# Kernel optimization log

Measured on AMD Instinct MI355X. Metric: run time of the kernel, lower is better.

The kernel has to match this reference:

```python
import jax, jax.numpy as jnp
import numpy as np
from jax import lax

B, T, U, V = 4, 200, 100, 1024
D_ENC, D_DEC, J = 144, 320, 320


def setup_inputs() -> dict:
    key = jax.random.key(0)
    ks = jax.random.split(key, 8)
    s = lambda d: 1.0 / np.sqrt(d).astype(np.float32)
    return {
        "enc_out": jax.random.normal(ks[0], (B, T, D_ENC), jnp.float32),
        "dec_out": jax.random.normal(ks[1], (B, U + 1, D_DEC), jnp.float32),
        "W_enc": jax.random.normal(ks[2], (D_ENC, J), jnp.float32) * s(D_ENC),
        "b_enc": jnp.zeros((J,), jnp.float32),
        "W_dec": jax.random.normal(ks[3], (D_DEC, J), jnp.float32) * s(D_DEC),
        "b_dec": jnp.zeros((J,), jnp.float32),
        "W_out": jax.random.normal(ks[4], (J, V), jnp.float32) * s(J),
        "b_out": jnp.zeros((V,), jnp.float32),
        "targets": jax.random.randint(ks[5], (B, U), 1, V, jnp.int32),
        "enc_lengths": jax.random.randint(ks[6], (B,), T // 2, T + 1, jnp.int32),
        "target_lengths": jax.random.randint(ks[7], (B,), U // 2, U + 1, jnp.int32),
    }


def _rnnt_loss(log_probs, targets, enc_lengths, target_lengths):
    # log_probs: [B, T, U+1, V]; blank index = 0 (matches RNNTLoss(blank=0))
    blank_lp = log_probs[..., 0]  # [B, T, U+1]
    idx = jnp.broadcast_to(targets[:, None, :, None].astype(jnp.int32), (B, T, U, 1))
    emit_lp = jnp.take_along_axis(log_probs[:, :, :U, :], idx, axis=-1)[..., 0]  # [B, T, U]

    # alpha[0, u] = sum of emit log-probs along u at t=0
    alpha0 = jnp.concatenate(
        [jnp.zeros((B, 1), log_probs.dtype), jnp.cumsum(emit_lp[:, 0, :], axis=1)], axis=1
    )  # [B, U+1]

    def row(a, emit_t):
        # a: alpha_prev + blank (vertical transitions), [B, U+1]; emit_t: [B, U]
        def step(prev, xs):
            a_u, e_prev = xs
            cur = jnp.logaddexp(a_u, prev + e_prev)
            return cur, cur
        _, rest = lax.scan(step, a[:, 0], (a[:, 1:].T, emit_t.T))  # rest: [U, B]
        return jnp.concatenate([a[:, :1], rest.T], axis=1)

    def t_step(alpha_prev, xs):
        blank_prev, emit_t = xs
        alpha_t = row(alpha_prev + blank_prev, emit_t)
        return alpha_t, alpha_t

    xs = (jnp.swapaxes(blank_lp[:, :-1, :], 0, 1), jnp.swapaxes(emit_lp[:, 1:, :], 0, 1))
    _, alphas_rest = lax.scan(t_step, alpha0, xs)  # [T-1, B, U+1]
    alphas = jnp.concatenate([alpha0[None], alphas_rest], axis=0)  # [T, B, U+1]

    b_idx = jnp.arange(B)
    t_idx = enc_lengths - 1
    ll = alphas[t_idx, b_idx, target_lengths] + blank_lp[b_idx, t_idx, target_lengths]
    return jnp.mean(-ll)  # reduction='mean' over batch


def reference(enc_out, dec_out, W_enc, b_enc, W_dec, b_dec, W_out, b_out, targets, enc_lengths, target_lengths):
    enc_p = enc_out @ W_enc + b_enc  # [B, T, J]
    dec_p = dec_out @ W_dec + b_dec  # [B, U+1, J]
    joint = jnp.tanh(enc_p[:, :, None, :] + dec_p[:, None, :, :])  # [B, T, U+1, J]
    logits = joint @ W_out + b_out  # [B, T, U+1, V]
    log_probs = jax.nn.log_softmax(logits, axis=-1)
    return _rnnt_loss(log_probs, targets, enc_lengths, target_lengths)
```

## Files before the change

kernel.cpp:

```cpp
#include <hip/hip_runtime.h>
#include <hip/hip_bf16.h>
#include <math.h>

#define B_ 4
#define T_ 200
#define U_ 100
#define V_ 1024
#define DE 144
#define DD 320
#define J_ 320
#define M_TOT (B_ * T_ * (U_ + 1))
#define SSTR 328
#define DSTR 104
#define NDIAG 300
#define LOG2E 1.4426950408889634f
#define LN2 0.6931471805599453f

typedef __attribute__((ext_vector_type(8))) short bf16x8_t;
typedef __attribute__((ext_vector_type(4))) float f32x4_t;

__device__ __forceinline__ float fast_tanh(float x) {
    float e = exp2f(x * (2.0f * LOG2E));
    float r = __frcp_rn(e + 1.0f);
    return fmaf(-2.0f, r, 1.0f);
}

__device__ __forceinline__ ushort f2bf(float x) {
    uint u = __float_as_uint(x);
    uint r = (u + 0x7FFFu + ((u >> 16) & 1u)) >> 16;
    return (ushort)r;
}

template <int K>
__device__ __forceinline__ void proj_body(const float* __restrict__ X,
                                          const float* __restrict__ W,
                                          const float* __restrict__ bias,
                                          float* __restrict__ Y,
                                          int r0, int R, float* sx, int tid) {
    constexpr int QK = K / 4;
    for (int q = tid; q < 16 * QK; q += 640) {
        int row = q / QK;
        int kq = q - row * QK;
        int r = r0 + row;
        if (r >= R) r = R - 1;
        *(float4*)&sx[row * K + kq * 4] = *(const float4*)&X[r * K + kq * 4];
    }
    __syncthreads();
    const int half = (tid >= 320) ? 1 : 0;
    const int c = tid - half * 320;
    float acc[8];
#pragma unroll
    for (int i = 0; i < 8; i++) acc[i] = 0.0f;
    for (int k = 0; k < K; k += 4) {
        float w0 = W[(k + 0) * 320 + c];
        float w1 = W[(k + 1) * 320 + c];
        float w2 = W[(k + 2) * 320 + c];
        float w3 = W[(k + 3) * 320 + c];
#pragma unroll
        for (int i = 0; i < 8; i++) {
            const float4 x4 = *(const float4*)&sx[(half * 8 + i) * K + k];
            acc[i] = fmaf(x4.x, w0, acc[i]);
            acc[i] = fmaf(x4.y, w1, acc[i]);
            acc[i] = fmaf(x4.z, w2, acc[i]);
            acc[i] = fmaf(x4.w, w3, acc[i]);
        }
    }
    const float bb = bias[c];
#pragma unroll
    for (int i = 0; i < 8; i++) {
        int r = r0 + half * 8 + i;
        if (r < R) Y[r * 320 + c] = acc[i] + bb;
    }
}

__global__ __launch_bounds__(640) void prep_kernel(
    const float* __restrict__ enc_out, const float* __restrict__ dec_out,
    const float* __restrict__ W_enc, const float* __restrict__ b_enc,
    const float* __restrict__ W_dec, const float* __restrict__ b_dec,
    const float* __restrict__ W_out,
    float* __restrict__ enc_p, float* __restrict__ dec_p,
    ushort* __restrict__ Wt) {
    __shared__ float sx[16 * 320];
    const int bid = blockIdx.x;
    const int tid = threadIdx.x;
    if (bid < 50) {
        proj_body<DE>(enc_out, W_enc, b_enc, enc_p, bid * 16, B_ * T_, sx, tid);
    } else if (bid < 76) {
        proj_body<DD>(dec_out, W_dec, b_dec, dec_p, (bid - 50) * 16,
                      B_ * (U_ + 1), sx, tid);
    } else {
        int idx = (bid - 76) * 640 + tid;
        int k = idx >> 10;
        int v = idx & 1023;
        ushort b = f2bf(W_out[idx]);
        int frag = (v >> 4) * 10 + (k >> 5);
        int lane = (v & 15) | (((k >> 3) & 3) << 4);
        int elem = k & 7;
        Wt[frag * 512 + lane * 8 + elem] = b;
    }
}

__global__ __launch_bounds__(1024, 4) void joint_mfma(
    const float* __restrict__ enc_p, const float* __restrict__ dec_p,
    const ushort* __restrict__ Wt, const float* __restrict__ b_out,
    const int* __restrict__ targets,
    float* __restrict__ bsk, float* __restrict__ esk) {
    __shared__ ushort sh[64 * SSTR];
    __shared__ float parts[16][64];
    __shared__ float lse_sh[64];
    __shared__ int tgt_sh[64];
    __shared__ int skb_sh[64];

    const int tid = threadIdx.x;
    const int r0 = blockIdx.x * 64;

    if (tid < 64) {
        int rc = r0 + tid;
        int tg = -1, skb = -1;
        if (rc < M_TOT) {
            int b = rc / 20200;
            int rem = rc - b * 20200;
            int t = rem / 101;
            int u = rem - t * 101;
            skb = (b * NDIAG + t + u) * DSTR + u;
            if (u < U_) tg = targets[b * U_ + u];
        }
        tgt_sh[tid] = tg;
        skb_sh[tid] = skb;
    }

    {
        const int si = tid >> 4;
        const int sq = tid & 15;
        int rc = r0 + si;
        if (rc > M_TOT - 1) rc = M_TOT - 1;
        int b = rc / 20200;
        int rem = rc - b * 20200;
        int t = rem / 101;
        int u = rem - t * 101;
        const float4* ep = (const float4*)&enc_p[(b * 200 + t) * 320];
        const float4* dp = (const float4*)&dec_p[(b * 101 + u) * 320];
        ushort* shp = &sh[si * SSTR];
#pragma unroll
        for (int it = 0; it < 5; it++) {
            int kq = sq + it * 16;
            float4 e = ep[kq];
            float4 dd = dp[kq];
            float t0 = fast_tanh(e.x + dd.x);
            float t1 = fast_tanh(e.y + dd.y);
            float t2 = fast_tanh(e.z + dd.z);
            float t3 = fast_tanh(e.w + dd.w);
            __hip_bfloat162 p0 = __float22bfloat162_rn(make_float2(t0, t1));
            __hip_bfloat162 p1 = __float22bfloat162_rn(make_float2(t2, t3));
            uint2 pk;
            pk.x = *(uint*)&p0;
            pk.y = *(uint*)&p1;
            *(uint2*)&shp[kq * 4] = pk;
        }
    }
    __syncthreads();

    const int wave = tid >> 6;
    const int lane = tid & 63;
    const int lrow = lane & 15;
    const int lk = (lane >> 4) * 8;
    const int cb16 = wave * 4;

    f32x4_t acc[4][4];
#pragma unroll
    for (int mt = 0; mt < 4; mt++)
#pragma unroll
        for (int nt = 0; nt < 4; nt++) acc[mt][nt] = (f32x4_t)(0.0f);

    for (int ks = 0; ks < 10; ks++) {
        bf16x8_t a[4];
#pragma unroll
        for (int mt = 0; mt < 4; mt++)
            a[mt] = *(const bf16x8_t*)&sh[(mt * 16 + lrow) * SSTR + ks * 32 + lk];
#pragma unroll
        for (int nt = 0; nt < 4; nt++) {
            bf16x8_t bfr = *(const bf16x8_t*)&Wt[(((cb16 + nt) * 10 + ks) << 9) + lane * 8];
            __builtin_amdgcn_s_setprio(1);
#pragma unroll
            for (int mt = 0; mt < 4; mt++)
                acc[mt][nt] = __builtin_amdgcn_mfma_f32_16x16x32_bf16(a[mt], bfr, acc[mt][nt], 0, 0, 0);
            __builtin_amdgcn_s_setprio(0);
        }
    }

    float bo[4];
#pragma unroll
    for (int nt = 0; nt < 4; nt++) bo[nt] = b_out[wave * 64 + nt * 16 + lrow];
#pragma unroll
    for (int mt = 0; mt < 4; mt++)
#pragma unroll
        for (int nt = 0; nt < 4; nt++) acc[mt][nt] += bo[nt];

#pragma unroll
    for (int mt = 0; mt < 4; mt++) {
#pragma unroll
        for (int j = 0; j < 4; j++) {
            float s = exp2f(acc[mt][0][j] * LOG2E);
            s += exp2f(acc[mt][1][j] * LOG2E);
            s += exp2f(acc[mt][2][j] * LOG2E);
            s += exp2f(acc[mt][3][j] * LOG2E);
#pragma unroll
            for (int off = 1; off < 16; off <<= 1)
                s += __shfl_xor(s, off, 16);
            if (lrow == 0) {
                int row = mt * 16 + (lane >> 4) * 4 + j;
                parts[wave][row] = s;
            }
        }
    }
    __syncthreads();
    if (tid < 64) {
        float s = parts[0][tid];
#pragma unroll
        for (int w = 1; w < 16; w++) s += parts[w][tid];
        lse_sh[tid] = __log2f(s) * LN2;
    }
    __syncthreads();

#pragma unroll
    for (int mt = 0; mt < 4; mt++) {
#pragma unroll
        for (int j = 0; j < 4; j++) {
            int lr = mt * 16 + (lane >> 4) * 4 + j;
            int skb = skb_sh[lr];
            if (skb < 0) continue;
            int tc = tgt_sh[lr];
            bool isblank = (wave == 0) && (lrow == 0);
            bool isemit = (tc >= 0) && ((tc >> 6) == wave) && ((tc & 15) == lrow);
            if (isblank || isemit) {
                float lse = lse_sh[lr];
                if (isblank) bsk[skb] = acc[mt][0][j] - lse;
                if (isemit) {
                    int ntl = (tc >> 4) & 3;
                    float v = acc[mt][0][j];
#pragma unroll
                    for (int nt = 1; nt < 4; nt++)
                        if (nt == ntl) v = acc[mt][nt][j];
                    esk[skb] = v - lse;
                }
            }
        }
    }
}

__global__ __launch_bounds__(256, 1) void alpha_c2_kernel(
    const float* __restrict__ bsk, const float* __restrict__ esk,
    const int* __restrict__ enc_len, const int* __restrict__ tgt_len,
    float* __restrict__ out) {
    __shared__ float ll_sh[B_];
    const int tid = threadIdx.x;
    const int b = tid >> 6;
    const int l = tid & 63;
    const float* Bp = bsk + b * (NDIAG * DSTR);
    const float* Ep = esk + b * (NDIAG * DSTR);
    const int el = enc_len[b];
    const int tl = tgt_len[b];
    const int dfin = el - 1 + tl;

    const int u0 = 2 * l;
    const bool ok0 = (u0 <= U_);
    const bool ok1 = (u0 + 1 <= U_);
    const int uc = ok0 ? u0 : 0;

    float A0 = (l == 0) ? 0.0f : -INFINITY;
    float A1 = -INFINITY;

    float2 rb[16], re[16];
#pragma unroll
    for (int k = 0; k < 16; k++) {
        rb[k] = *(const float2*)&Bp[k * DSTR + uc];
        re[k] = *(const float2*)&Ep[k * DSTR + uc];
    }

    for (int dc = 1; dc <= 289; dc += 16) {
#pragma unroll
        for (int q = 0; q < 16; q++) {
            const int d = dc + q;
            if (d > NDIAG - 1) continue;
            const int sc = q;
            const int sm = (q + 1) & 15;
            float2 cb = rb[sc], ce = re[sc];
            float2 mb = rb[sm];
            int dn = d + 15;
            if (dn > NDIAG - 1) dn = NDIAG - 1;
            rb[sc] = *(const float2*)&Bp[dn * DSTR + uc];
            re[sc] = *(const float2*)&Ep[dn * DSTR + uc];

            float s = A1 + ce.y;
            float sn = __shfl_up(s, 1, 64);

            float va0 = A0 + cb.x;
            float vb0 = (l >= 1) ? sn : -INFINITY;
            float va1 = A1 + cb.y;
            float vb1 = A0 + ce.x;

            float M0 = fmaxf(va0, vb0);
            float n0 = (M0 == -INFINITY)
                           ? -INFINITY
                           : M0 + __logf(1.0f + __expf(fminf(va0, vb0) - M0));
            float M1 = fmaxf(va1, vb1);
            float n1 = (M1 == -INFINITY)
                           ? -INFINITY
                           : M1 + __logf(1.0f + __expf(fminf(va1, vb1) - M1));

            const int t0 = d - u0;
            if (!ok0 || t0 < 0 || t0 >= T_) n0 = -INFINITY;
            if (!ok1 || (t0 - 1) < 0 || (t0 - 1) >= T_) n1 = -INFINITY;

            if (d == dfin) {
                if (tl == u0) ll_sh[b] = n0 + mb.x;
                if (tl == u0 + 1) ll_sh[b] = n1 + mb.y;
            }
            A0 = n0;
            A1 = n1;
        }
    }
    __syncthreads();
    if (tid == 0)
        out[0] = -0.25f * (ll_sh[0] + ll_sh[1] + ll_sh[2] + ll_sh[3]);
}

extern "C" void kernel_launch(void* const* d_in, const int* in_sizes, int n_in,
                              void* d_out, int out_size, void* d_ws, size_t ws_size,
                              hipStream_t stream) {
    const float* enc_out = (const float*)d_in[0];
    const float* dec_out = (const float*)d_in[1];
    const float* W_enc = (const float*)d_in[2];
    const float* b_enc = (const float*)d_in[3];
    const float* W_dec = (const float*)d_in[4];
    const float* b_dec = (const float*)d_in[5];
    const float* W_out = (const float*)d_in[6];
    const float* b_out = (const float*)d_in[7];
    const int* targets = (const int*)d_in[8];
    const int* enc_len = (const int*)d_in[9];
    const int* tgt_len = (const int*)d_in[10];

    float* ws = (float*)d_ws;
    float* enc_p = ws;
    float* dec_p = enc_p + B_ * T_ * J_;
    float* bsk = dec_p + B_ * (U_ + 1) * J_;
    float* esk = bsk + B_ * NDIAG * DSTR;
    ushort* Wt = (ushort*)(esk + B_ * NDIAG * DSTR);

    prep_kernel<<<588, 640, 0, stream>>>(enc_out, dec_out, W_enc, b_enc,
                                         W_dec, b_dec, W_out, enc_p, dec_p, Wt);

    joint_mfma<<<(M_TOT + 63) / 64, 1024, 0, stream>>>(
        enc_p, dec_p, Wt, b_out, targets, bsk, esk);

    alpha_c2_kernel<<<1, 256, 0, stream>>>(bsk, esk, enc_len, tgt_len,
                                           (float*)d_out);
}
```

Measured before the change: 204.4 us.

## Fuse prep, joint GEMM and alpha recursion into one cooperative persistent kernel

Replaces three kernel launches with a single cooperative kernel of 256 persistent blocks. Grid syncs separate the projection/weight-conversion phase, a grid-stride loop over joint GEMM tiles, and the alpha recursion run by one block. It also folds the output bias into the exp2 FMA argument. The aim is to remove launch overhead and inter-kernel gaps. In exchange, the GEMM phase runs at only 256 blocks, which may lower occupancy, and the grid-wide barriers add their own cost.

```diff
diff --git a/kernel.cpp b/kernel.cpp
--- a/kernel.cpp
+++ b/kernel.cpp
@@ -1,6 +1,9 @@
 #include <hip/hip_runtime.h>
 #include <hip/hip_bf16.h>
+#include <hip/hip_cooperative_groups.h>
 #include <math.h>
+
+namespace cg = cooperative_groups;
 
 #define B_ 4
 #define T_ 200
@@ -10,6 +13,7 @@
 #define DD 320
 #define J_ 320
 #define M_TOT (B_ * T_ * (U_ + 1))
+#define NTILES 1263
 #define SSTR 328
 #define DSTR 104
 #define NDIAG 300
@@ -31,298 +35,293 @@
     return (ushort)r;
 }
 
-template <int K>
-__device__ __forceinline__ void proj_body(const float* __restrict__ X,
-                                          const float* __restrict__ W,
-                                          const float* __restrict__ bias,
-                                          float* __restrict__ Y,
-                                          int r0, int R, float* sx, int tid) {
-    constexpr int QK = K / 4;
-    for (int q = tid; q < 16 * QK; q += 640) {
-        int row = q / QK;
-        int kq = q - row * QK;
-        int r = r0 + row;
-        if (r >= R) r = R - 1;
-        *(float4*)&sx[row * K + kq * 4] = *(const float4*)&X[r * K + kq * 4];
-    }
-    __syncthreads();
-    const int half = (tid >= 320) ? 1 : 0;
-    const int c = tid - half * 320;
-    float acc[8];
-#pragma unroll
-    for (int i = 0; i < 8; i++) acc[i] = 0.0f;
-    for (int k = 0; k < K; k += 4) {
-        float w0 = W[(k + 0) * 320 + c];
-        float w1 = W[(k + 1) * 320 + c];
-        float w2 = W[(k + 2) * 320 + c];
-        float w3 = W[(k + 3) * 320 + c];
-#pragma unroll
-        for (int i = 0; i < 8; i++) {
-            const float4 x4 = *(const float4*)&sx[(half * 8 + i) * K + k];
-            acc[i] = fmaf(x4.x, w0, acc[i]);
-            acc[i] = fmaf(x4.y, w1, acc[i]);
-            acc[i] = fmaf(x4.z, w2, acc[i]);
-            acc[i] = fmaf(x4.w, w3, acc[i]);
-        }
-    }
-    const float bb = bias[c];
-#pragma unroll
-    for (int i = 0; i < 8; i++) {
-        int r = r0 + half * 8 + i;
-        if (r < R) Y[r * 320 + c] = acc[i] + bb;
-    }
-}
-
-__global__ __launch_bounds__(640) void prep_kernel(
+__global__ __launch_bounds__(1024, 4) void fused_kernel(
     const float* __restrict__ enc_out, const float* __restrict__ dec_out,
     const float* __restrict__ W_enc, const float* __restrict__ b_enc,
     const float* __restrict__ W_dec, const float* __restrict__ b_dec,
-    const float* __restrict__ W_out,
+    const float* __restrict__ W_out, const float* __restrict__ b_out,
+    const int* __restrict__ targets, const int* __restrict__ enc_len,
+    const int* __restrict__ tgt_len,
     float* __restrict__ enc_p, float* __restrict__ dec_p,
-    ushort* __restrict__ Wt) {
-    __shared__ float sx[16 * 320];
-    const int bid = blockIdx.x;
-    const int tid = threadIdx.x;
-    if (bid < 50) {
-        proj_body<DE>(enc_out, W_enc, b_enc, enc_p, bid * 16, B_ * T_, sx, tid);
-    } else if (bid < 76) {
-        proj_body<DD>(dec_out, W_dec, b_dec, dec_p, (bid - 50) * 16,
-                      B_ * (U_ + 1), sx, tid);
-    } else {
-        int idx = (bid - 76) * 640 + tid;
-        int k = idx >> 10;
-        int v = idx & 1023;
-        ushort b = f2bf(W_out[idx]);
-        int frag = (v >> 4) * 10 + (k >> 5);
-        int lane = (v & 15) | (((k >> 3) & 3) << 4);
-        int elem = k & 7;
-        Wt[frag * 512 + lane * 8 + elem] = b;
-    }
-}
-
-__global__ __launch_bounds__(1024, 4) void joint_mfma(
-    const float* __restrict__ enc_p, const float* __restrict__ dec_p,
-    const ushort* __restrict__ Wt, const float* __restrict__ b_out,
-    const int* __restrict__ targets,
-    float* __restrict__ bsk, float* __restrict__ esk) {
-    __shared__ ushort sh[64 * SSTR];
+    float* __restrict__ bsk, float* __restrict__ esk,
+    ushort* __restrict__ Wt, float* __restrict__ out) {
+    __shared__ __align__(16) ushort sh[64 * SSTR];
     __shared__ float parts[16][64];
     __shared__ float lse_sh[64];
     __shared__ int tgt_sh[64];
     __shared__ int skb_sh[64];
-
+    __shared__ float ll_sh[B_];
+
+    cg::grid_group grid = cg::this_grid();
+    const int bid = blockIdx.x;
     const int tid = threadIdx.x;
-    const int r0 = blockIdx.x * 64;
-
-    if (tid < 64) {
-        int rc = r0 + tid;
-        int tg = -1, skb = -1;
-        if (rc < M_TOT) {
-            int b = rc / 20200;
-            int rem = rc - b * 20200;
-            int t = rem / 101;
-            int u = rem - t * 101;
-            skb = (b * NDIAG + t + u) * DSTR + u;
-            if (u < U_) tg = targets[b * U_ + u];
-        }
-        tgt_sh[tid] = tg;
-        skb_sh[tid] = skb;
+
+    if (bid < 76) {
+        const float* X; const float* W; const float* bias; float* Y;
+        int K, r0, R;
+        if (bid < 50) { X = enc_out; W = W_enc; bias = b_enc; Y = enc_p;
+                        K = DE; r0 = bid * 16; R = B_ * T_; }
+        else          { X = dec_out; W = W_dec; bias = b_dec; Y = dec_p;
+                        K = DD; r0 = (bid - 50) * 16; R = B_ * (U_ + 1); }
+        float* sx = (float*)sh;
+        const int QK = K >> 2;
+        for (int q = tid; q < 16 * QK; q += 1024) {
+            int row = q / QK;
+            int kq = q - row * QK;
+            int r = r0 + row;
+            if (r >= R) r = R - 1;
+            *(float4*)&sx[row * K + kq * 4] = *(const float4*)&X[r * K + kq * 4];
+        }
+        __syncthreads();
+        if (tid < 640) {
+            const int half = (tid >= 320) ? 1 : 0;
+            const int c = tid - half * 320;
+            float acc[8];
+#pragma unroll
+            for (int i = 0; i < 8; i++) acc[i] = 0.0f;
+            for (int k = 0; k < K; k += 4) {
+                float w0 = W[(k + 0) * 320 + c];
+                float w1 = W[(k + 1) * 320 + c];
+                float w2 = W[(k + 2) * 320 + c];
+                float w3 = W[(k + 3) * 320 + c];
+#pragma unroll
+                for (int i = 0; i < 8; i++) {
+                    const float4 x4 = *(const float4*)&sx[(half * 8 + i) * K + k];
+                    acc[i] = fmaf(x4.x, w0, acc[i]);
+                    acc[i] = fmaf(x4.y, w1, acc[i]);
+                    acc[i] = fmaf(x4.z, w2, acc[i]);
+                    acc[i] = fmaf(x4.w, w3, acc[i]);
+                }
+            }
+            const float bb = bias[c];
+#pragma unroll
+            for (int i = 0; i < 8; i++) {
+                int r = r0 + half * 8 + i;
+                if (r < R) Y[r * 320 + c] = acc[i] + bb;
+            }
+        }
+    } else {
+        for (int idx = (bid - 76) * 1024 + tid; idx < J_ * V_; idx += 180 * 1024) {
+            int k = idx >> 10;
+            int v = idx & 1023;
+            ushort b = f2bf(W_out[idx]);
+            int frag = (v >> 4) * 10 + (k >> 5);
+            int lane = (v & 15) | (((k >> 3) & 3) << 4);
+            Wt[frag * 512 + lane * 8 + (k & 7)] = b;
+        }
     }
-
-    {
-        const int si = tid >> 4;
-        const int sq = tid & 15;
-        int rc = r0 + si;
-        if (rc > M_TOT - 1) rc = M_TOT - 1;
-        int b = rc / 20200;
-        int rem = rc - b * 20200;
-        int t = rem / 101;
-        int u = rem - t * 101;
-        const float4* ep = (const float4*)&enc_p[(b * 200 + t) * 320];
-        const float4* dp = (const float4*)&dec_p[(b * 101 + u) * 320];
-        ushort* shp = &sh[si * SSTR];
-#pragma unroll
-        for (int it = 0; it < 5; it++) {
-            int kq = sq + it * 16;
-            float4 e = ep[kq];
-            float4 dd = dp[kq];
-            float t0 = fast_tanh(e.x + dd.x);
-            float t1 = fast_tanh(e.y + dd.y);
-            float t2 = fast_tanh(e.z + dd.z);
-            float t3 = fast_tanh(e.w + dd.w);
-            __hip_bfloat162 p0 = __float22bfloat162_rn(make_float2(t0, t1));
-            __hip_bfloat162 p1 = __float22bfloat162_rn(make_float2(t2, t3));
-            uint2 pk;
-            pk.x = *(uint*)&p0;
-            pk.y = *(uint*)&p1;
-            *(uint2*)&shp[kq * 4] = pk;
-        }
-    }
-    __syncthreads();
+    grid.sync();
 
     const int wave = tid >> 6;
     const int lane = tid & 63;
     const int lrow = lane & 15;
     const int lk = (lane >> 4) * 8;
     const int cb16 = wave * 4;
-
-    f32x4_t acc[4][4];
-#pragma unroll
-    for (int mt = 0; mt < 4; mt++)
-#pragma unroll
-        for (int nt = 0; nt < 4; nt++) acc[mt][nt] = (f32x4_t)(0.0f);
-
-    for (int ks = 0; ks < 10; ks++) {
-        bf16x8_t a[4];
+    float bo4[4], boL[4];
+#pragma unroll
+    for (int nt = 0; nt < 4; nt++) {
+        float b = b_out[wave * 64 + nt * 16 + lrow];
+        bo4[nt] = b;
+        boL[nt] = b * LOG2E;
+    }
+
+    for (int tile = bid; tile < NTILES; tile += 256) {
+        const int r0 = tile * 64;
+
+        if (tid < 64) {
+            int rc = r0 + tid;
+            int tg = -1, skb = -1;
+            if (rc < M_TOT) {
+                int b = rc / 20200;
+                int rem = rc - b * 20200;
+                int t = rem / 101;
+                int u = rem - t * 101;
+                skb = (b * NDIAG + t + u) * DSTR + u;
+                if (u < U_) tg = targets[b * U_ + u];
+            }
+            tgt_sh[tid] = tg;
+            skb_sh[tid] = skb;
+        }
+        {
+            const int si = tid >> 4;
+            const int sq = tid & 15;
+            int rc = r0 + si;
+            if (rc > M_TOT - 1) rc = M_TOT - 1;
+            int b = rc / 20200;
+            int rem = rc - b * 20200;
+            int t = rem / 101;
+            int u = rem - t * 101;
+            const float4* ep = (const float4*)&enc_p[(b * 200 + t) * 320];
+            const float4* dp = (const float4*)&dec_p[(b * 101 + u) * 320];
+            ushort* shp = &sh[si * SSTR];
+#pragma unroll
+            for (int it = 0; it < 5; it++) {
+                int kq = sq + it * 16;
+                float4 e = ep[kq];
+                float4 dd = dp[kq];
+                float t0 = fast_tanh(e.x + dd.x);
+                float t1 = fast_tanh(e.y + dd.y);
+                float t2 = fast_tanh(e.z + dd.z);
+                float t3 = fast_tanh(e.w + dd.w);
+                __hip_bfloat162 p0 = __float22bfloat162_rn(make_float2(t0, t1));
+                __hip_bfloat162 p1 = __float22bfloat162_rn(make_float2(t2, t3));
+                uint2 pk;
+                pk.x = *(uint*)&p0;
+                pk.y = *(uint*)&p1;
+                *(uint2*)&shp[kq * 4] = pk;
+            }
+        }
+        __syncthreads();
+
+        f32x4_t acc[4][4];
 #pragma unroll
         for (int mt = 0; mt < 4; mt++)
-            a[mt] = *(const bf16x8_t*)&sh[(mt * 16 + lrow) * SSTR + ks * 32 + lk];
-#pragma unroll
-        for (int nt = 0; nt < 4; nt++) {
-            bf16x8_t bfr = *(const bf16x8_t*)&Wt[(((cb16 + nt) * 10 + ks) << 9) + lane * 8];
-            __builtin_amdgcn_s_setprio(1);
+#pragma unroll
+            for (int nt = 0; nt < 4; nt++) acc[mt][nt] = (f32x4_t)(0.0f);
+
+        for (int ks = 0; ks < 10; ks++) {
+            bf16x8_t a[4];
 #pragma unroll
             for (int mt = 0; mt < 4; mt++)
-                acc[mt][nt] = __builtin_amdgcn_mfma_f32_16x16x32_bf16(a[mt], bfr, acc[mt][nt], 0, 0, 0);
-            __builtin_amdgcn_s_setprio(0);
-        }
+                a[mt] = *(const bf16x8_t*)&sh[(mt * 16 + lrow) * SSTR + ks * 32 + lk];
+#pragma unroll
+            for (int nt = 0; nt < 4; nt++) {
+                bf16x8_t bfr = *(const bf16x8_t*)&Wt[(((cb16 + nt) * 10 + ks) << 9) + lane * 8];
+                __builtin_amdgcn_s_setprio(1);
+#pragma unroll
+                for (int mt = 0; mt < 4; mt++)
+                    acc[mt][nt] = __builtin_amdgcn_mfma_f32_16x16x32_bf16(a[mt], bfr, acc[mt][nt], 0, 0, 0);
+                __builtin_amdgcn_s_setprio(0);
+            }
+        }
+
+#pragma unroll
+        for (int mt = 0; mt < 4; mt++) {
+#pragma unroll
+            for (int j = 0; j < 4; j++) {
+                float s = exp2f(fmaf(acc[mt][0][j], LOG2E, boL[0]));
+                s += exp2f(fmaf(acc[mt][1][j], LOG2E, boL[1]));
+                s += exp2f(fmaf(acc[mt][2][j], LOG2E, boL[2]));
+                s += exp2f(fmaf(acc[mt][3][j], LOG2E, boL[3]));
+#pragma unroll
+                for (int off = 1; off < 16; off <<= 1)
+                    s += __shfl_xor(s, off, 16);
+                if (lrow == 0) {
+                    int row = mt * 16 + (lane >> 4) * 4 + j;
+                    parts[wave][row] = s;
+                }
+            }
+        }
+        __syncthreads();
+        if (tid < 64) {
+            float s = parts[0][tid];
+#pragma unroll
+            for (int w = 1; w < 16; w++) s += parts[w][tid];
+            lse_sh[tid] = __log2f(s) * LN2;
+        }
+        __syncthreads();
+
+#pragma unroll
+        for (int mt = 0; mt < 4; mt++) {
+#pragma unroll
+            for (int j = 0; j < 4; j++) {
+                int lr = mt * 16 + (lane >> 4) * 4 + j;
+                int skb = skb_sh[lr];
+                if (skb < 0) continue;
+                int tc = tgt_sh[lr];
+                bool isblank = (wave == 0) && (lrow == 0);
+                bool isemit = (tc >= 0) && ((tc >> 6) == wave) && ((tc & 15) == lrow);
+                if (isblank || isemit) {
+                    float lse = lse_sh[lr];
+                    if (isblank) bsk[skb] = acc[mt][0][j] + bo4[0] - lse;
+                    if (isemit) {
+                        int ntl = (tc >> 4) & 3;
+                        float v = acc[mt][0][j] + bo4[0];
+#pragma unroll
+                        for (int nt = 1; nt < 4; nt++)
+                            if (nt == ntl) v = acc[mt][nt][j] + bo4[nt];
+                        esk[skb] = v - lse;
+                    }
+                }
+            }
+        }
+        __syncthreads();
     }
-
-    float bo[4];
-#pragma unroll
-    for (int nt = 0; nt < 4; nt++) bo[nt] = b_out[wave * 64 + nt * 16 + lrow];
-#pragma unroll
-    for (int mt = 0; mt < 4; mt++)
-#pragma unroll
-        for (int nt = 0; nt < 4; nt++) acc[mt][nt] += bo[nt];
-
-#pragma unroll
-    for (int mt = 0; mt < 4; mt++) {
-#pragma unroll
-        for (int j = 0; j < 4; j++) {
-            float s = exp2f(acc[mt][0][j] * LOG2E);
-            s += exp2f(acc[mt][1][j] * LOG2E);
-            s += exp2f(acc[mt][2][j] * LOG2E);
-            s += exp2f(acc[mt][3][j] * LOG2E);
-#pragma unroll
-            for (int off = 1; off < 16; off <<= 1)
-                s += __shfl_xor(s, off, 16);
-            if (lrow == 0) {
-                int row = mt * 16 + (lane >> 4) * 4 + j;
-                parts[wave][row] = s;
-            }
-        }
+    grid.sync();
+
+    if (bid == 255) {
+        if (tid < 256) {
+            const int b = tid >> 6;
+            const int l = tid & 63;
+            const float* Bp = bsk + b * (NDIAG * DSTR);
+            const float* Ep = esk + b * (NDIAG * DSTR);
+            const int el = enc_len[b];
+            const int tl = tgt_len[b];
+            const int dfin = el - 1 + tl;
+
+            const int u0 = 2 * l;
+            const bool ok0 = (u0 <= U_);
+            const bool ok1 = (u0 + 1 <= U_);
+            const int uc = ok0 ? u0 : 0;
+
+            float A0 = (l == 0) ? 0.0f : -INFINITY;
+            float A1 = -INFINITY;
+
+            float2 rb[16], re[16];
+#pragma unroll
+            for (int k = 0; k < 16; k++) {
+                rb[k] = *(const float2*)&Bp[k * DSTR + uc];
+                re[k] = *(const float2*)&Ep[k * DSTR + uc];
+            }
+
+            for (int dc = 1; dc <= 289; dc += 16) {
+#pragma unroll
+                for (int q = 0; q < 16; q++) {
+                    const int d = dc + q;
+                    if (d > NDIAG - 1) continue;
+                    const int sc = q;
+                    const int sm = (q + 1) & 15;
+                    float2 cb = rb[sc], ce = re[sc];
+                    float2 mb = rb[sm];
+                    int dn = d + 15;
+                    if (dn > NDIAG - 1) dn = NDIAG - 1;
+                    rb[sc] = *(const float2*)&Bp[dn * DSTR + uc];
+                    re[sc] = *(const float2*)&Ep[dn * DSTR + uc];
+
+                    float s = A1 + ce.y;
+                    float sn = __shfl_up(s, 1, 64);
+
+                    float va0 = A0 + cb.x;
+                    float vb0 = (l >= 1) ? sn : -INFINITY;
+                    float va1 = A1 + cb.y;
+                    float vb1 = A0 + ce.x;
+
+                    float M0 = fmaxf(va0, vb0);
+                    float n0 = (M0 == -INFINITY)
+                                   ? -INFINITY
+                                   : M0 + __logf(1.0f + __expf(fminf(va0, vb0) - M0));
+                    float M1 = fmaxf(va1, vb1);
+                    float n1 = (M1 == -INFINITY)
+                                   ? -INFINITY
+                                   : M1 + __logf(1.0f + __expf(fminf(va1, vb1) - M1));
+
+                    const int t0 = d - u0;
+                    if (!ok0 || t0 < 0 || t0 >= T_) n0 = -INFINITY;
+                    if (!ok1 || (t0 - 1) < 0 || (t0 - 1) >= T_) n1 = -INFINITY;
+
+                    if (d == dfin) {
+                        if (tl == u0) ll_sh[b] = n0 + mb.x;
+                        if (tl == u0 + 1) ll_sh[b] = n1 + mb.y;
+                    }
+                    A0 = n0;
+                    A1 = n1;
+                }
+            }
+        }
+        __syncthreads();
+        if (tid == 0)
+            out[0] = -0.25f * (ll_sh[0] + ll_sh[1] + ll_sh[2] + ll_sh[3]);
     }
-    __syncthreads();
-    if (tid < 64) {
-        float s = parts[0][tid];
-#pragma unroll
-        for (int w = 1; w < 16; w++) s += parts[w][tid];
-        lse_sh[tid] = __log2f(s) * LN2;
-    }
-    __syncthreads();
-
-#pragma unroll
-    for (int mt = 0; mt < 4; mt++) {
-#pragma unroll
-        for (int j = 0; j < 4; j++) {
-            int lr = mt * 16 + (lane >> 4) * 4 + j;
-            int skb = skb_sh[lr];
-            if (skb < 0) continue;
-            int tc = tgt_sh[lr];
-            bool isblank = (wave == 0) && (lrow == 0);
-            bool isemit = (tc >= 0) && ((tc >> 6) == wave) && ((tc & 15) == lrow);
-            if (isblank || isemit) {
-                float lse = lse_sh[lr];
-                if (isblank) bsk[skb] = acc[mt][0][j] - lse;
-                if (isemit) {
-                    int ntl = (tc >> 4) & 3;
-                    float v = acc[mt][0][j];
-#pragma unroll
-                    for (int nt = 1; nt < 4; nt++)
-                        if (nt == ntl) v = acc[mt][nt][j];
-                    esk[skb] = v - lse;
-                }
-            }
-        }
-    }
-}
-
-__global__ __launch_bounds__(256, 1) void alpha_c2_kernel(
-    const float* __restrict__ bsk, const float* __restrict__ esk,
-    const int* __restrict__ enc_len, const int* __restrict__ tgt_len,
-    float* __restrict__ out) {
-    __shared__ float ll_sh[B_];
-    const int tid = threadIdx.x;
-    const int b = tid >> 6;
-    const int l = tid & 63;
-    const float* Bp = bsk + b * (NDIAG * DSTR);
-    const float* Ep = esk + b * (NDIAG * DSTR);
-    const int el = enc_len[b];
-    const int tl = tgt_len[b];
-    const int dfin = el - 1 + tl;
-
-    const int u0 = 2 * l;
-    const bool ok0 = (u0 <= U_);
-    const bool ok1 = (u0 + 1 <= U_);
-    const int uc = ok0 ? u0 : 0;
-
-    float A0 = (l == 0) ? 0.0f : -INFINITY;
-    float A1 = -INFINITY;
-
-    float2 rb[16], re[16];
-#pragma unroll
-    for (int k = 0; k < 16; k++) {
-        rb[k] = *(const float2*)&Bp[k * DSTR + uc];
-        re[k] = *(const float2*)&Ep[k * DSTR + uc];
-    }
-
-    for (int dc = 1; dc <= 289; dc += 16) {
-#pragma unroll
-        for (int q = 0; q < 16; q++) {
-            const int d = dc + q;
-            if (d > NDIAG - 1) continue;
-            const int sc = q;
-            const int sm = (q + 1) & 15;
-            float2 cb = rb[sc], ce = re[sc];
-            float2 mb = rb[sm];
-            int dn = d + 15;
-            if (dn > NDIAG - 1) dn = NDIAG - 1;
-            rb[sc] = *(const float2*)&Bp[dn * DSTR + uc];
-            re[sc] = *(const float2*)&Ep[dn * DSTR + uc];
-
-            float s = A1 + ce.y;
-            float sn = __shfl_up(s, 1, 64);
-
-            float va0 = A0 + cb.x;
-            float vb0 = (l >= 1) ? sn : -INFINITY;
-            float va1 = A1 + cb.y;
-            float vb1 = A0 + ce.x;
-
-            float M0 = fmaxf(va0, vb0);
-            float n0 = (M0 == -INFINITY)
-                           ? -INFINITY
-                           : M0 + __logf(1.0f + __expf(fminf(va0, vb0) - M0));
-            float M1 = fmaxf(va1, vb1);
-            float n1 = (M1 == -INFINITY)
-                           ? -INFINITY
-                           : M1 + __logf(1.0f + __expf(fminf(va1, vb1) - M1));
-
-            const int t0 = d - u0;
-            if (!ok0 || t0 < 0 || t0 >= T_) n0 = -INFINITY;
-            if (!ok1 || (t0 - 1) < 0 || (t0 - 1) >= T_) n1 = -INFINITY;
-
-            if (d == dfin) {
-                if (tl == u0) ll_sh[b] = n0 + mb.x;
-                if (tl == u0 + 1) ll_sh[b] = n1 + mb.y;
-            }
-            A0 = n0;
-            A1 = n1;
-        }
-    }
-    __syncthreads();
-    if (tid == 0)
-        out[0] = -0.25f * (ll_sh[0] + ll_sh[1] + ll_sh[2] + ll_sh[3]);
 }
 
 extern "C" void kernel_launch(void* const* d_in, const int* in_sizes, int n_in,
@@ -346,13 +345,14 @@
     float* bsk = dec_p + B_ * (U_ + 1) * J_;
     float* esk = bsk + B_ * NDIAG * DSTR;
     ushort* Wt = (ushort*)(esk + B_ * NDIAG * DSTR);
-
-    prep_kernel<<<588, 640, 0, stream>>>(enc_out, dec_out, W_enc, b_enc,
-                                         W_dec, b_dec, W_out, enc_p, dec_p, Wt);
-
-    joint_mfma<<<(M_TOT + 63) / 64, 1024, 0, stream>>>(
-        enc_p, dec_p, Wt, b_out, targets, bsk, esk);
-
-    alpha_c2_kernel<<<1, 256, 0, stream>>>(bsk, esk, enc_len, tgt_len,
-                                           (float*)d_out);
+    float* outp = (float*)d_out;
+
+    void* args[] = {(void*)&enc_out, (void*)&dec_out, (void*)&W_enc,
+                    (void*)&b_enc,   (void*)&W_dec,   (void*)&b_dec,
+                    (void*)&W_out,   (void*)&b_out,   (void*)&targets,
+                    (void*)&enc_len, (void*)&tgt_len, (void*)&enc_p,
+                    (void*)&dec_p,   (void*)&bsk,     (void*)&esk,
+                    (void*)&Wt,      (void*)&outp};
+    hipLaunchCooperativeKernel((const void*)fused_kernel, dim3(256), dim3(1024),
+                               args, 0, stream);
 }
```

Result: slower. 365.8 us (+78.9%).
